# Kernel optimization log

Hardware: AMD Instinct MI355X
Metric: run time of the kernel (lower is better)

The kernel has to match this reference:

```python
import jax, jax.numpy as jnp
import numpy as np

N_FFT = 512
HOP = 128
WIN_LENGTH = 512  # == n_fft, so no window padding needed


def hann_periodic(n):
    # torch.hann_window default is periodic=True
    return (0.5 - 0.5 * jnp.cos(2.0 * jnp.pi * jnp.arange(n) / n)).astype(jnp.float32)


def setup_inputs() -> dict:
    key = jax.random.key(0)
    k1, _ = jax.random.split(key)
    B, C, F, T = 16, 2, N_FFT // 2 + 1, 2048
    X = jax.random.normal(k1, (B, C, F, T, 2), dtype=jnp.float32)
    window = hann_periodic(WIN_LENGTH)
    return {"X": X, "window": window}


def istft(X, window):
    # X: (B, C, F, T, 2) real+imag; onesided, center=True, normalized=False
    Xc = jax.lax.complex(X[..., 0], X[..., 1])          # (B, C, F, T)
    frames = jnp.fft.irfft(Xc, n=N_FFT, axis=-2)        # (B, C, n_fft, T)
    frames = frames * window[None, None, :, None]       # windowed frames
    frames = jnp.moveaxis(frames, -2, -1)               # (B, C, T, n_fft)

    T = frames.shape[-2]
    full_len = N_FFT + (T - 1) * HOP
    # overlap-add scatter indices: (T, n_fft)
    idx = (jnp.arange(T) * HOP)[:, None] + jnp.arange(N_FFT)[None, :]

    y = jnp.zeros(frames.shape[:2] + (full_len,), frames.dtype).at[..., idx].add(frames)
    # window-envelope normalization (sum of squared windows, overlap-added)
    env = jnp.zeros((full_len,), window.dtype).at[idx].add(
        jnp.broadcast_to(window * window, (T, N_FFT)))

    pad = N_FFT // 2  # center=True trims n_fft//2 from both ends
    return y[..., pad:full_len - pad] / env[pad:full_len - pad]


def reference(X, window):
    return istft(X, window)  # (B, C, (T-1)*hop)
```

## Files before the change

### kernel.cpp

```cpp
#include <hip/hip_runtime.h>
#include <hip/hip_bf16.h>

#define NFFT    512
#define HOPSZ   128
#define FBINS   257
#define TFR     2048
#define NBC     32
#define OUTLEN  262016
#define SPAD    256

typedef __bf16 bf16x8 __attribute__((ext_vector_type(8)));
typedef float  f32x4  __attribute__((ext_vector_type(4)));

static __device__ __forceinline__ float bf2f(unsigned short u) {
    union { unsigned int i; float f; } x; x.i = (unsigned int)u << 16; return x.f;
}

__device__ __forceinline__ void gld_lds16(const void* g, void* l) {
    __builtin_amdgcn_global_load_lds(
        (const __attribute__((address_space(1))) unsigned int*)g,
        (__attribute__((address_space(3))) unsigned int*)l, 16, 0, 0);
}

__global__ __launch_bounds__(256) void k_wgen(const float* __restrict__ wnd,
                                              uint4* __restrict__ Wf) {
    const int gid  = blockIdx.x * 256 + threadIdx.x;
    const int lane = gid & 63;
    const int rt   = (gid >> 6) & 31;
    const int ks   = gid >> 11;
    const int n    = rt * 16 + (lane & 15);
    const int kb   = ks * 32 + ((lane >> 4) << 2);
    const float wn = wnd[n] * (1.0f / 512.0f);
    union { uint4 u; unsigned short h[8]; } o;
    #pragma unroll
    for (int j = 0; j < 8; ++j) {
        const int k = kb + (j & 3) + 16 * (j >> 2);
        float val = 0.0f;
        if (k < 2 * FBINS) {
            const int f = k >> 1;
            const bool edge = (f == 0) || (f == 256);
            const float cf = edge ? 1.0f : 2.0f;
            const int m = (f * n) & (NFFT - 1);
            const float ang = (float)m * 0.01227184630308513f;
            float s, c;
            __sincosf(ang, &s, &c);
            val = (k & 1) ? (edge ? 0.0f : -cf * wn * s) : (cf * wn * c);
        }
        __hip_bfloat16 hb = __float2bfloat16(val);
        o.h[j] = *(unsigned short*)&hb;
    }
    Wf[gid] = o.u;
}

__global__ __launch_bounds__(512, 4) void k_mm(
    const float* __restrict__ X,
    const uint4* __restrict__ Wf,
    __hip_bfloat16* __restrict__ frames)
{
    __shared__ uint4 Ab[2][32][64];
    __shared__ uint4 Bb[2][4][4][16];

    const int tid  = threadIdx.x;
    const int lane = tid & 63;
    const int w    = tid >> 6;
    const int q    = lane >> 4;
    const int rlo  = lane & 15;

    const int bid = blockIdx.x;
    const int id  = (bid & 7) * 128 + (bid >> 3);
    const int bc  = id >> 5;
    const int t0b = (id & 31) << 6;

    const float2* __restrict__ X2 = (const float2*)X + (size_t)bc * FBINS * TFR;

    const int sf  = tid >> 5;
    const int stt = tid & 31;
    const int sq  = ((2 * sf) & 15) >> 2;
    const int sjw = (sf & 1) + 2 * (sf >> 3);
    unsigned int* __restrict__ BbU = (unsigned int*)Bb;

    f32x4  acc[4][4] = {};
    float2 xvA[2], xvB[2];

    auto issueA = [&](int ks, int buf) {
        const uint4* src = Wf + (size_t)ks * 2048;
        uint4* dst = &Ab[buf][0][0];
        #pragma unroll
        for (int r = 0; r < 4; ++r)
            gld_lds16(src + r * 512 + tid, dst + r * 512 + tid);
    };
    auto issueB = [&](int ks, float2* xv) {
        const float2* xb = X2 + (size_t)(ks * 16 + sf) * TFR + t0b + stt;
        xv[0] = xb[0];
        xv[1] = xb[32];
    };
    auto packB = [&](int buf, float2* xv) {
        #pragma unroll
        for (int d = 0; d < 2; ++d) {
            union { unsigned int u; __hip_bfloat16 h[2]; } p;
            p.h[0] = __float2bfloat16(xv[d].x);
            p.h[1] = __float2bfloat16(xv[d].y);
            const int tile = (stt >> 4) + 2 * d;
            BbU[((((buf * 4 + sq) * 4 + tile) * 16) + (stt & 15)) * 4 + sjw] = p.u;
        }
    };
    auto compute = [&](int buf) {
        uint4 a[4], b[4];
        #pragma unroll
        for (int ni = 0; ni < 4; ++ni) b[ni] = Bb[buf][q][ni][rlo];
        #pragma unroll
        for (int mi = 0; mi < 4; ++mi) a[mi] = Ab[buf][4 * w + mi][lane];
        #pragma unroll
        for (int mi = 0; mi < 4; ++mi)
            #pragma unroll
            for (int ni = 0; ni < 4; ++ni)
                acc[mi][ni] = __builtin_amdgcn_mfma_f32_16x16x32_bf16(
                    __builtin_bit_cast(bf16x8, a[mi]),
                    __builtin_bit_cast(bf16x8, b[ni]), acc[mi][ni], 0, 0, 0);
    };

    issueB(0, xvA);
    issueA(0, 0);
    packB(0, xvA);
    __syncthreads();

    #pragma unroll
    for (int ks = 0; ks < 16; ++ks) {
        const int cur = ks & 1;
        if (ks < 15) {
            if (ks & 1) issueB(ks + 1, xvA); else issueB(ks + 1, xvB);
            issueA(ks + 1, cur ^ 1);
        }
        compute(cur);
        if (ks < 15) {
            if (ks & 1) packB(cur ^ 1, xvA); else packB(cur ^ 1, xvB);
            __syncthreads();
        }
    }

    unsigned short* fb = (unsigned short*)frames;
    #pragma unroll
    for (int mi = 0; mi < 4; ++mi) {
        const int nbase = (w << 6) + (mi << 4) + (q << 2);
        #pragma unroll
        for (int ni = 0; ni < 4; ++ni) {
            const int t = t0b + ni * 16 + rlo;
            union { ushort4 u; __hip_bfloat16 hh[4]; } pk;
            pk.hh[0] = __float2bfloat16(acc[mi][ni][0]);
            pk.hh[1] = __float2bfloat16(acc[mi][ni][1]);
            pk.hh[2] = __float2bfloat16(acc[mi][ni][2]);
            pk.hh[3] = __float2bfloat16(acc[mi][ni][3]);
            *(ushort4*)(fb + (((size_t)(bc * TFR + t)) << 9) + nbase) = pk.u;
        }
    }
}

__global__ __launch_bounds__(256) void k_ola(
    const __hip_bfloat16* __restrict__ frames,
    const float* __restrict__ wnd,
    const float* __restrict__ X,
    float* __restrict__ out)
{
    const int bc = blockIdx.y;
    const int o  = (blockIdx.x * 256 + threadIdx.x) * 4;
    if (o >= OUTLEN) return;
    const int s   = o + SPAD;
    const int tb_ = s >> 7;
    const int nb  = s & (HOPSZ - 1);
    const unsigned short* fb = (const unsigned short*)frames + (size_t)bc * TFR * NFFT;
    const float* Xre = X + (((size_t)bc * FBINS + 256) * TFR) * 2;
    const float sA = ((nb & 1) ? -1.0f : 1.0f) * (1.0f / 512.0f);
    float y0 = 0.f, y1 = 0.f, y2 = 0.f, y3 = 0.f;
    float e0 = 0.f, e1 = 0.f, e2 = 0.f, e3 = 0.f;
    #pragma unroll
    for (int r = 0; r < 4; ++r) {
        const int t = tb_ - r;
        if ((unsigned)t > (unsigned)(TFR - 1)) continue;
        const int n = nb + (r << 7);
        ushort4 v = *(const ushort4*)(fb + (size_t)t * NFFT + n);
        float4  wv = *(const float4*)(wnd + n);
        const float c = sA * Xre[2 * t];
        y0 += bf2f(v.x) + c * wv.x; e0 += wv.x * wv.x;
        y1 += bf2f(v.y) - c * wv.y; e1 += wv.y * wv.y;
        y2 += bf2f(v.z) + c * wv.z; e2 += wv.z * wv.z;
        y3 += bf2f(v.w) - c * wv.w; e3 += wv.w * wv.w;
    }
    float4 res = make_float4(y0 / e0, y1 / e1, y2 / e2, y3 / e3);
    *(float4*)(out + (size_t)bc * OUTLEN + o) = res;
}

extern "C" void kernel_launch(void* const* d_in, const int* in_sizes, int n_in,
                              void* d_out, int out_size, void* d_ws, size_t ws_size,
                              hipStream_t stream) {
    (void)in_sizes; (void)n_in; (void)out_size; (void)ws_size;
    const float* X   = (const float*)d_in[0];
    const float* wnd = (const float*)d_in[1];
    float* out = (float*)d_out;

    uint4* Wf = (uint4*)d_ws;
    __hip_bfloat16* frames = (__hip_bfloat16*)((char*)d_ws + (1 << 20));

    k_wgen<<<136, 256, 0, stream>>>(wnd, Wf);
    k_mm<<<1024, 512, 0, stream>>>(X, Wf, frames);
    k_ola<<<dim3((OUTLEN / 4 + 255) / 256, NBC), 256, 0, stream>>>(frames, wnd, X, out);
}
```

Baseline: 85.81 us.

## Retile GEMM blocks to 256x128 with 4x2 warp grid and M-split

Changes the frame-synthesis GEMM block tile from 512 samples x 64 frames to 256 samples x 128 frames, pairing two blocks per 128-frame panel that each take one half of the basis matrix. Warps are arranged 4x2 over the tile, and the B staging is reorganized so each thread loads two frequency rows and packs them into 8-byte LDS writes. Each block now reads and converts twice the input spectrum columns while loading half the basis matrix per k-step. The trade-off is that X is read twice across the block pair, while the per-block LDS traffic for A is halved.

New measurement: 82.51 us. -3.8%, faster.

```diff
diff --git a/kernel.cpp b/kernel.cpp
--- a/kernel.cpp
+++ b/kernel.cpp
@@ -57,59 +57,62 @@
     const uint4* __restrict__ Wf,
     __hip_bfloat16* __restrict__ frames)
 {
-    __shared__ uint4 Ab[2][32][64];
-    __shared__ uint4 Bb[2][4][4][16];
+    __shared__ uint4 Ab[2][1024];
+    __shared__ uint4 Bb[2][4][128];
 
     const int tid  = threadIdx.x;
     const int lane = tid & 63;
     const int w    = tid >> 6;
+    const int wr   = w >> 1;
+    const int wc   = w & 1;
     const int q    = lane >> 4;
     const int rlo  = lane & 15;
 
     const int bid = blockIdx.x;
     const int id  = (bid & 7) * 128 + (bid >> 3);
-    const int bc  = id >> 5;
-    const int t0b = (id & 31) << 6;
+    const int m     = id & 1;
+    const int pair  = id >> 1;
+    const int panel = pair & 15;
+    const int bc    = pair >> 4;
+    const int t0b   = panel << 7;
 
     const float2* __restrict__ X2 = (const float2*)X + (size_t)bc * FBINS * TFR;
 
-    const int sf  = tid >> 5;
-    const int stt = tid & 31;
-    const int sq  = ((2 * sf) & 15) >> 2;
-    const int sjw = (sf & 1) + 2 * (sf >> 3);
-    unsigned int* __restrict__ BbU = (unsigned int*)Bb;
+    const int p  = tid >> 6;
+    const int st = tid & 63;
+    const int sq = p & 3;
+    const int sh = p >> 2;
 
     f32x4  acc[4][4] = {};
-    float2 xvA[2], xvB[2];
+    float2 xv[2][4];
 
     auto issueA = [&](int ks, int buf) {
-        const uint4* src = Wf + (size_t)ks * 2048;
-        uint4* dst = &Ab[buf][0][0];
-        #pragma unroll
-        for (int r = 0; r < 4; ++r)
-            gld_lds16(src + r * 512 + tid, dst + r * 512 + tid);
-    };
-    auto issueB = [&](int ks, float2* xv) {
-        const float2* xb = X2 + (size_t)(ks * 16 + sf) * TFR + t0b + stt;
-        xv[0] = xb[0];
-        xv[1] = xb[32];
-    };
-    auto packB = [&](int buf, float2* xv) {
-        #pragma unroll
-        for (int d = 0; d < 2; ++d) {
-            union { unsigned int u; __hip_bfloat16 h[2]; } p;
-            p.h[0] = __float2bfloat16(xv[d].x);
-            p.h[1] = __float2bfloat16(xv[d].y);
-            const int tile = (stt >> 4) + 2 * d;
-            BbU[((((buf * 4 + sq) * 4 + tile) * 16) + (stt & 15)) * 4 + sjw] = p.u;
-        }
+        const uint4* src = Wf + (size_t)ks * 2048 + m * 1024;
+        gld_lds16(src + tid,       &Ab[buf][tid]);
+        gld_lds16(src + 512 + tid, &Ab[buf][512 + tid]);
+    };
+    auto issueB = [&](int ks, float2 (&bx)[4]) {
+        const float2* xb = X2 + (size_t)(ks * 16 + 2 * p) * TFR + t0b + st;
+        bx[0] = xb[0];
+        bx[1] = xb[TFR];
+        bx[2] = xb[64];
+        bx[3] = xb[TFR + 64];
+    };
+    auto packB = [&](int buf, float2 (&bx)[4]) {
+        union { uint2 u; __hip_bfloat16 hh[4]; } p0, p1;
+        p0.hh[0] = __float2bfloat16(bx[0].x); p0.hh[1] = __float2bfloat16(bx[0].y);
+        p0.hh[2] = __float2bfloat16(bx[1].x); p0.hh[3] = __float2bfloat16(bx[1].y);
+        p1.hh[0] = __float2bfloat16(bx[2].x); p1.hh[1] = __float2bfloat16(bx[2].y);
+        p1.hh[2] = __float2bfloat16(bx[3].x); p1.hh[3] = __float2bfloat16(bx[3].y);
+        ((uint2*)&Bb[buf][sq][st])[sh]      = p0.u;
+        ((uint2*)&Bb[buf][sq][st + 64])[sh] = p1.u;
     };
     auto compute = [&](int buf) {
         uint4 a[4], b[4];
         #pragma unroll
-        for (int ni = 0; ni < 4; ++ni) b[ni] = Bb[buf][q][ni][rlo];
-        #pragma unroll
-        for (int mi = 0; mi < 4; ++mi) a[mi] = Ab[buf][4 * w + mi][lane];
+        for (int ni = 0; ni < 4; ++ni) b[ni] = Bb[buf][q][wc * 64 + ni * 16 + rlo];
+        #pragma unroll
+        for (int mi = 0; mi < 4; ++mi) a[mi] = Ab[buf][(4 * wr + mi) * 64 + lane];
         #pragma unroll
         for (int mi = 0; mi < 4; ++mi)
             #pragma unroll
@@ -119,21 +122,21 @@
                     __builtin_bit_cast(bf16x8, b[ni]), acc[mi][ni], 0, 0, 0);
     };
 
-    issueB(0, xvA);
+    issueB(0, xv[0]);
     issueA(0, 0);
-    packB(0, xvA);
+    packB(0, xv[0]);
     __syncthreads();
 
     #pragma unroll
     for (int ks = 0; ks < 16; ++ks) {
         const int cur = ks & 1;
         if (ks < 15) {
-            if (ks & 1) issueB(ks + 1, xvA); else issueB(ks + 1, xvB);
+            issueB(ks + 1, xv[(ks + 1) & 1]);
             issueA(ks + 1, cur ^ 1);
         }
         compute(cur);
         if (ks < 15) {
-            if (ks & 1) packB(cur ^ 1, xvA); else packB(cur ^ 1, xvB);
+            packB(cur ^ 1, xv[(ks + 1) & 1]);
             __syncthreads();
         }
     }
@@ -141,10 +144,10 @@
     unsigned short* fb = (unsigned short*)frames;
     #pragma unroll
     for (int mi = 0; mi < 4; ++mi) {
-        const int nbase = (w << 6) + (mi << 4) + (q << 2);
+        const int nbase = m * 256 + wr * 64 + mi * 16 + (q << 2);
         #pragma unroll
         for (int ni = 0; ni < 4; ++ni) {
-            const int t = t0b + ni * 16 + rlo;
+            const int t = t0b + wc * 64 + ni * 16 + rlo;
             union { ushort4 u; __hip_bfloat16 hh[4]; } pk;
             pk.hh[0] = __float2bfloat16(acc[mi][ni][0]);
             pk.hh[1] = __float2bfloat16(acc[mi][ni][1]);
```
